# Performance work log

Hardware: AMD Instinct MI355X
Metric: run time of the kernel (lower is better)

The kernel has to match this reference:

```python
import jax, jax.numpy as jnp
import numpy as np

_EPSILON = 1e-6

def _sparsemax(z):
    # sparsemax along last axis. z: [b, m]
    z_sorted = -jnp.sort(-z, axis=-1)                       # descending sort
    m = z.shape[-1]
    k = jnp.arange(1, m + 1, dtype=z.dtype)                 # [m]
    z_cumsum = jnp.cumsum(z_sorted, axis=-1)                # [b, m]
    support = (1.0 + k * z_sorted) > z_cumsum               # [b, m] bool
    k_z = jnp.sum(support, axis=-1, keepdims=True)          # [b, 1] int, size of support
    cs_at_k = jnp.take_along_axis(z_cumsum, k_z - 1, axis=-1)
    tau = (cs_at_k - 1.0) / k_z.astype(z.dtype)             # threshold
    return jnp.maximum(z - tau, 0.0)


def setup_inputs() -> dict:
    key = jax.random.key(0)
    ks = jax.random.split(key, 6)
    b, m, dim, out_dim = 4096, 8192, 1024, 1000
    encoder_output = jax.random.normal(ks[0], (b, dim), dtype=jnp.float32)
    memory_set = jax.random.normal(ks[1], (m, dim), dtype=jnp.float32)
    loss_weights = jax.random.uniform(ks[2], (m, 1), dtype=jnp.float32)
    # classifier: Linear(2*dim, 4*dim) -> ReLU -> Linear(4*dim, out_dim)
    W1 = jax.random.normal(ks[3], (4 * dim, 2 * dim), dtype=jnp.float32) * (1.0 / np.sqrt(2 * dim))
    b1 = jnp.zeros((4 * dim,), dtype=jnp.float32)
    W2 = jax.random.normal(ks[4], (out_dim, 4 * dim), dtype=jnp.float32) * (1.0 / np.sqrt(4 * dim))
    b2 = jnp.zeros((out_dim,), dtype=jnp.float32)
    return {"encoder_output": encoder_output, "memory_set": memory_set,
            "loss_weights": loss_weights, "W1": W1, "b1": b1, "W2": W2, "b2": b2}


def reference(encoder_output, memory_set, loss_weights, W1, b1, W2, b2):
    # cosine distance: d = 1 - x_norm @ y_norm^T
    x_norm = encoder_output * jax.lax.rsqrt(
        jnp.sum(encoder_output * encoder_output, axis=1, keepdims=True) + _EPSILON)
    y_norm = memory_set * jax.lax.rsqrt(
        jnp.sum(memory_set * memory_set, axis=1, keepdims=True) + _EPSILON)
    d = 1.0 - jnp.matmul(x_norm, y_norm.T)                  # [b, m]
    content_weights = _sparsemax(-d)                        # [b, m], sparse rows
    memory_vector = jnp.matmul(content_weights, memory_set) # [b, dim]
    final_input = jnp.concatenate([encoder_output, memory_vector], axis=1)  # [b, 2*dim]
    h = jax.nn.relu(jnp.matmul(final_input, W1.T) + b1)
    output = jnp.matmul(h, W2.T) + b2                       # [b, out_dim]
    return output
```

## Files before the change

### kernel.cpp

```cpp
#include <hip/hip_runtime.h>

typedef __bf16 bf16;
typedef __bf16 bf16x4 __attribute__((ext_vector_type(4)));
typedef __bf16 bf16x8 __attribute__((ext_vector_type(8)));
typedef float f32x4 __attribute__((ext_vector_type(4)));
typedef _Float16 f16x8 __attribute__((ext_vector_type(8)));
typedef unsigned short ushort4v __attribute__((ext_vector_type(4)));

#define WS_OFF_S    (0ull)
#define WS_OFF_P4   (67108864ull)
#define WS_OFF_MB   (134217728ull)
#define WS_OFF_W1B  (150994944ull)
#define WS_OFF_W2B  (167772160ull)
#define WS_OFF_FI   (176160768ull)
#define WS_OFF_XN   (192937984ull)
#define WS_OFF_YN   (201326592ull)
#define WS_OFF_H    (0ull)

__device__ __forceinline__ void gload_lds16(const void* g, void* l) {
  __builtin_amdgcn_global_load_lds(
      (const __attribute__((address_space(1))) void*)g,
      (__attribute__((address_space(3))) void*)l, 16, 0, 0);
}

__device__ __forceinline__ f32x4 bf4_to_f32(bf16x4 v) {
  const ushort4v u = __builtin_bit_cast(ushort4v, v);
  f32x4 r;
#pragma unroll
  for (int k = 0; k < 4; ++k) {
    const unsigned q = ((unsigned)u[k]) << 16;
    r[k] = __builtin_bit_cast(float, q);
  }
  return r;
}

__device__ __forceinline__ float f16bits_to_f32(unsigned hb) {
  return (float)__builtin_bit_cast(_Float16, (unsigned short)hb);
}

template<int EPI>
__global__ __launch_bounds__(512, 2)
void gemm_nt256(const bf16* __restrict__ A, const bf16* __restrict__ B,
                void* __restrict__ Cout, const float* __restrict__ bias,
                int K, int ldab, int ldc)
{
  __shared__ alignas(16) bf16 As[2][256 * 64];
  __shared__ alignas(16) bf16 Bs[2][256 * 64];
  const int tid  = threadIdx.x;
  const int lane = tid & 63;
  const int wave = tid >> 6;
  const int wr = wave >> 2, wc = wave & 3;
  const int gx  = gridDim.x;
  const int nwg = gx * gridDim.y;
  int flat = blockIdx.y * gx + blockIdx.x;
  flat = (flat & 7) * (nwg >> 3) + (flat >> 3);
  const int bm0 = (flat / gx) << 8;
  const int bn0 = (flat % gx) << 8;
  const int zc  = blockIdx.z;

  const int lr    = lane >> 3;
  const int scolb = ((lane & 7) << 4) ^ (lr << 4);
  const int row0  = (wave << 5) + lr;
  const char* Ag = (const char*)(A + (size_t)(bm0 + row0) * ldab + (size_t)zc * K) + scolb;
  const char* Bg = (const char*)(B + (size_t)(bn0 + row0) * ldab + (size_t)zc * K) + scolb;
  char* Alds = (char*)As + (wave << 12);
  char* Blds = (char*)Bs + (wave << 12);
  const size_t rstride8 = (size_t)16 * ldab;

  int offA[2][8], offB[2][4];
  const int kb = (lane >> 4) << 4;
#pragma unroll
  for (int ks = 0; ks < 2; ++ks) {
#pragma unroll
    for (int m = 0; m < 8; ++m) {
      const int rA = (wr << 7) + (m << 4) + (lane & 15);
      offA[ks][m] = (rA << 7) + ((((ks << 6) + kb)) ^ ((rA & 7) << 4));
    }
#pragma unroll
    for (int n = 0; n < 4; ++n) {
      const int rB = (wc << 6) + (n << 4) + (lane & 15);
      offB[ks][n] = (rB << 7) + ((((ks << 6) + kb)) ^ ((rB & 7) << 4));
    }
  }

  f32x4 acc[8][4];
#pragma unroll
  for (int m = 0; m < 8; ++m)
#pragma unroll
    for (int n = 0; n < 4; ++n) acc[m][n] = (f32x4)(0.0f);

  auto STAGE = [&](int buf) {
    char* Ad = Alds + (buf << 15);
    char* Bd = Blds + (buf << 15);
#pragma unroll
    for (int i = 0; i < 4; ++i) gload_lds16(Ag + i * rstride8, Ad + (i << 10));
#pragma unroll
    for (int i = 0; i < 4; ++i) gload_lds16(Bg + i * rstride8, Bd + (i << 10));
    Ag += 128; Bg += 128;
  };

  const int nt = K >> 6;
  STAGE(0);
  STAGE(1);
  int cur = 0;
  for (int t = 0; t < nt; ++t) {
    if (t + 1 < nt) { asm volatile("s_waitcnt vmcnt(8)" ::: "memory"); }
    else            { asm volatile("s_waitcnt vmcnt(0)" ::: "memory"); }
    __builtin_amdgcn_s_barrier();
    asm volatile("" ::: "memory");
    const char* Ab = (const char*)As + (cur << 15);
    const char* Bb = (const char*)Bs + (cur << 15);
    __builtin_amdgcn_s_setprio(1);
#pragma unroll
    for (int ks = 0; ks < 2; ++ks) {
      bf16x8 av[8], bv[4];
#pragma unroll
      for (int m = 0; m < 8; ++m) av[m] = *(const bf16x8*)(Ab + offA[ks][m]);
#pragma unroll
      for (int n = 0; n < 4; ++n) bv[n] = *(const bf16x8*)(Bb + offB[ks][n]);
#pragma unroll
      for (int m = 0; m < 8; ++m)
#pragma unroll
        for (int n = 0; n < 4; ++n)
          acc[m][n] = __builtin_amdgcn_mfma_f32_16x16x32_bf16(av[m], bv[n], acc[m][n], 0, 0, 0);
    }
    __builtin_amdgcn_s_setprio(0);
    asm volatile("" ::: "memory");
    __builtin_amdgcn_s_barrier();
    if (t + 2 < nt) STAGE(cur);
    cur ^= 1;
  }

  const int r0 = bm0 + (wr << 7) + ((lane >> 4) << 2);
  const int c0 = bn0 + (wc << 6) + (lane & 15);
#pragma unroll
  for (int m = 0; m < 8; ++m) {
#pragma unroll
    for (int n = 0; n < 4; ++n) {
      const int col = c0 + (n << 4);
#pragma unroll
      for (int j = 0; j < 4; ++j) {
        const int row = r0 + (m << 4) + j;
        const float v = acc[m][n][j];
        if (EPI == 0) {
          ((_Float16*)Cout)[(size_t)row * ldc + col] = (_Float16)v;
        } else if (EPI == 2) {
          float t2 = v + bias[col];
          t2 = t2 > 0.f ? t2 : 0.f;
          ((bf16*)Cout)[(size_t)row * ldc + col] = (bf16)t2;
        } else {
          ((float*)Cout)[((size_t)zc << 22) + (size_t)row * ldc + col] = v;
        }
      }
    }
  }
}

__global__ __launch_bounds__(256)
void reduce_bias_kernel(const float* __restrict__ P4, const float* __restrict__ b2,
                        float* __restrict__ out)
{
  const int row = blockIdx.x;
  const int t = threadIdx.x;
  if (t >= 250) return;
  const size_t base = (size_t)row * 1024 + (t << 2);
  const float4 p0 = *(const float4*)(P4 + base);
  const float4 p1 = *(const float4*)(P4 + base + (1ull << 22));
  const float4 p2 = *(const float4*)(P4 + base + (2ull << 22));
  const float4 p3 = *(const float4*)(P4 + base + (3ull << 22));
  const float4 bb = ((const float4*)b2)[t];
  float4 r;
  r.x = p0.x + p1.x + p2.x + p3.x + bb.x;
  r.y = p0.y + p1.y + p2.y + p3.y + bb.y;
  r.z = p0.z + p1.z + p2.z + p3.z + bb.z;
  r.w = p0.w + p1.w + p2.w + p3.w + bb.w;
  *(float4*)(out + (size_t)row * 1000 + (t << 2)) = r;
}

__global__ __launch_bounds__(256)
void rownorm_kernel(const float* __restrict__ X, bf16* __restrict__ XN,
                    bf16* __restrict__ RAW, int ldraw)
{
  const int row = blockIdx.x;
  const int tid = threadIdx.x;
  const float4 v = ((const float4*)(X + (size_t)row * 1024))[tid];
  float ss = v.x * v.x + v.y * v.y + v.z * v.z + v.w * v.w;
#pragma unroll
  for (int o = 32; o > 0; o >>= 1) ss += __shfl_down(ss, o);
  __shared__ float red[4];
  if ((tid & 63) == 0) red[tid >> 6] = ss;
  __syncthreads();
  const float rn = rsqrtf(red[0] + red[1] + red[2] + red[3] + 1e-6f);
  union { bf16 h[4]; unsigned long long u; } p;
  p.h[0] = (bf16)(v.x * rn); p.h[1] = (bf16)(v.y * rn);
  p.h[2] = (bf16)(v.z * rn); p.h[3] = (bf16)(v.w * rn);
  ((unsigned long long*)(XN + (size_t)row * 1024))[tid] = p.u;
  if (RAW != nullptr) {
    union { bf16 h[4]; unsigned long long u; } q;
    q.h[0] = (bf16)v.x; q.h[1] = (bf16)v.y; q.h[2] = (bf16)v.z; q.h[3] = (bf16)v.w;
    ((unsigned long long*)(RAW + (size_t)row * ldraw))[tid] = q.u;
  }
}

__global__ void cvt_bf16_kernel(const float* __restrict__ src, bf16* __restrict__ dst, int n4) {
  const int i = blockIdx.x * blockDim.x + threadIdx.x;
  if (i >= n4) return;
  const float4 v = ((const float4*)src)[i];
  union { bf16 h[4]; unsigned long long u; } p;
  p.h[0] = (bf16)v.x; p.h[1] = (bf16)v.y; p.h[2] = (bf16)v.z; p.h[3] = (bf16)v.w;
  ((unsigned long long*)dst)[i] = p.u;
}

__global__ void cvt_w2_kernel(const float* __restrict__ src, bf16* __restrict__ dst) {
  const int i = blockIdx.x * blockDim.x + threadIdx.x;
  const int row = i >> 10;
  union { bf16 h[4]; unsigned long long u; } p;
  if (row < 1000) {
    const float4 v = ((const float4*)src)[i];
    p.h[0] = (bf16)v.x; p.h[1] = (bf16)v.y; p.h[2] = (bf16)v.z; p.h[3] = (bf16)v.w;
  } else {
    p.u = 0ull;
  }
  ((unsigned long long*)dst)[i] = p.u;
}

#define LCAP 1024
__global__ __launch_bounds__(256, 4)
void sparsemax_gather_kernel(const _Float16* __restrict__ S, const bf16* __restrict__ MB,
                             bf16* __restrict__ FI)
{
  const int row = blockIdx.x;
  const int tid = threadIdx.x;
  const f16x8* zs = (const f16x8*)(S + (size_t)row * 8192);
  float z[32];
  float lsum = 0.f;
#pragma unroll
  for (int t = 0; t < 4; ++t) {
    const f16x8 v = zs[t * 256 + tid];
#pragma unroll
    for (int j = 0; j < 8; ++j) { const float f = (float)v[j]; z[t * 8 + j] = f; lsum += f; }
  }
#pragma unroll
  for (int b = 0; b < 32; ++b) asm volatile("" : "+v"(z[b]));

  __shared__ float redS[4], redC[4];
  __shared__ unsigned pbuf[LCAP];
  __shared__ int lcnt;
  float s = lsum;
#pragma unroll
  for (int o = 32; o > 0; o >>= 1) s += __shfl_down(s, o);
  if ((tid & 63) == 0) redS[tid >> 6] = s;
  __syncthreads();
  float tau = (redS[0] + redS[1] + redS[2] + redS[3] - 1.0f) * (1.0f / 8192.0f);

  for (int it = 0; it < 64; ++it) {
    float ls = 0.f, lc = 0.f;
#pragma unroll
    for (int j = 0; j < 32; ++j) {
      const float v = z[j];
      if (v > tau) { ls += v; lc += 1.0f; }
    }
#pragma unroll
    for (int o = 32; o > 0; o >>= 1) { ls += __shfl_down(ls, o); lc += __shfl_down(lc, o); }
    __syncthreads();
    if ((tid & 63) == 0) { redS[tid >> 6] = ls; redC[tid >> 6] = lc; }
    __syncthreads();
    const float Ssum = redS[0] + redS[1] + redS[2] + redS[3];
    const float Csum = redC[0] + redC[1] + redC[2] + redC[3];
    const float ntau = (Ssum - 1.0f) / Csum;
    if (!(ntau > tau)) break;
    tau = ntau;
  }

  unsigned pend = 0;
#pragma unroll
  for (int b = 0; b < 32; ++b)
    if (z[b] > tau) pend |= (1u << b);

  const bf16* MBt = MB + (tid << 2);
  f32x4 acc0 = (f32x4)(0.0f), acc1 = (f32x4)(0.0f);
  for (;;) {
    if (tid == 0) lcnt = 0;
    __syncthreads();
#pragma unroll
    for (int b = 0; b < 32; ++b) {
      if (pend & (1u << b)) {
        const int slot = atomicAdd(&lcnt, 1);
        if (slot < LCAP) {
          const unsigned short wb =
              __builtin_bit_cast(unsigned short, (_Float16)(z[b] - tau));
          const unsigned idx = (unsigned)((((b >> 3) * 256 + tid) << 3) + (b & 7));
          pbuf[slot] = ((unsigned)wb << 16) | idx;
          pend &= ~(1u << b);
        }
      }
    }
    __syncthreads();
    const int nb = min(lcnt, LCAP);
    int e = 0;
    for (; e + 1 < nb; e += 2) {
      const uint2 pk2 = *(const uint2*)&pbuf[e];
      const float w0 = f16bits_to_f32(pk2.x >> 16);
      const float w1 = f16bits_to_f32(pk2.y >> 16);
      const bf16x4 v0 = *(const bf16x4*)(MBt + ((size_t)(pk2.x & 0xffffu) << 10));
      const bf16x4 v1 = *(const bf16x4*)(MBt + ((size_t)(pk2.y & 0xffffu) << 10));
      acc0 += bf4_to_f32(v0) * w0;
      acc1 += bf4_to_f32(v1) * w1;
    }
    if (e < nb) {
      const unsigned pk = pbuf[e];
      const float w = f16bits_to_f32(pk >> 16);
      const bf16x4 v = *(const bf16x4*)(MBt + ((size_t)(pk & 0xffffu) << 10));
      acc0 += bf4_to_f32(v) * w;
    }
    if (!__syncthreads_or(pend != 0)) break;
  }

  const f32x4 acc = acc0 + acc1;
  union { bf16 h[4]; unsigned long long u; } p;
  p.h[0] = (bf16)acc[0]; p.h[1] = (bf16)acc[1];
  p.h[2] = (bf16)acc[2]; p.h[3] = (bf16)acc[3];
  ((unsigned long long*)(FI + (size_t)row * 2048 + 1024))[tid] = p.u;
}

extern "C" void kernel_launch(void* const* d_in, const int* in_sizes, int n_in,
                              void* d_out, int out_size, void* d_ws, size_t ws_size,
                              hipStream_t stream)
{
  const float* enc = (const float*)d_in[0];
  const float* mem = (const float*)d_in[1];
  const float* W1  = (const float*)d_in[3];
  const float* b1  = (const float*)d_in[4];
  const float* W2  = (const float*)d_in[5];
  const float* b2  = (const float*)d_in[6];
  float* out = (float*)d_out;
  char* ws = (char*)d_ws;

  _Float16* S = (_Float16*)(ws + WS_OFF_S);
  float* P4 = (float*)(ws + WS_OFF_P4);
  bf16* MB  = (bf16*)(ws + WS_OFF_MB);
  bf16* W1B = (bf16*)(ws + WS_OFF_W1B);
  bf16* W2B = (bf16*)(ws + WS_OFF_W2B);
  bf16* FI  = (bf16*)(ws + WS_OFF_FI);
  bf16* XN  = (bf16*)(ws + WS_OFF_XN);
  bf16* YN  = (bf16*)(ws + WS_OFF_YN);
  bf16* H   = (bf16*)(ws + WS_OFF_H);

  rownorm_kernel<<<4096, 256, 0, stream>>>(enc, XN, FI, 2048);
  rownorm_kernel<<<8192, 256, 0, stream>>>(mem, YN, MB, 1024);
  cvt_bf16_kernel<<<8192, 256, 0, stream>>>(W1, W1B, 2097152);
  cvt_w2_kernel<<<4096, 256, 0, stream>>>(W2, W2B);

  gemm_nt256<0><<<dim3(32, 16), 512, 0, stream>>>(XN, YN, S, nullptr, 1024, 1024, 8192);
  sparsemax_gather_kernel<<<4096, 256, 0, stream>>>(S, MB, FI);
  gemm_nt256<2><<<dim3(16, 16), 512, 0, stream>>>(FI, W1B, H, b1, 2048, 2048, 4096);
  gemm_nt256<4><<<dim3(4, 16, 4), 512, 0, stream>>>(H, W2B, P4, nullptr, 1024, 4096, 1024);
  reduce_bias_kernel<<<4096, 256, 0, stream>>>(P4, b2, out);
}
```

Measured before the change: 447.7 us.

## Stage sparsemax row in LDS and warm-start tau from mean/std estimate

Measured after the change: 454.0 us. No clear change (+1.4%).

```diff
diff --git a/kernel.cpp b/kernel.cpp
--- a/kernel.cpp
+++ b/kernel.cpp
@@ -225,40 +225,50 @@
 }
 
 #define LCAP 1024
-__global__ __launch_bounds__(256, 4)
+__global__ __launch_bounds__(256, 6)
 void sparsemax_gather_kernel(const _Float16* __restrict__ S, const bf16* __restrict__ MB,
                              bf16* __restrict__ FI)
 {
   const int row = blockIdx.x;
   const int tid = threadIdx.x;
+
+  __shared__ alignas(16) unsigned short zl[8192];
+  __shared__ alignas(16) unsigned pbuf[LCAP];
+  __shared__ float redS[4], redC[4];
+  __shared__ int lcnt;
+  f16x8* zl8 = (f16x8*)zl;
+
   const f16x8* zs = (const f16x8*)(S + (size_t)row * 8192);
-  float z[32];
-  float lsum = 0.f;
+  float s1 = 0.f, s2 = 0.f;
 #pragma unroll
   for (int t = 0; t < 4; ++t) {
     const f16x8 v = zs[t * 256 + tid];
-#pragma unroll
-    for (int j = 0; j < 8; ++j) { const float f = (float)v[j]; z[t * 8 + j] = f; lsum += f; }
-  }
-#pragma unroll
-  for (int b = 0; b < 32; ++b) asm volatile("" : "+v"(z[b]));
-
-  __shared__ float redS[4], redC[4];
-  __shared__ unsigned pbuf[LCAP];
-  __shared__ int lcnt;
-  float s = lsum;
-#pragma unroll
-  for (int o = 32; o > 0; o >>= 1) s += __shfl_down(s, o);
-  if ((tid & 63) == 0) redS[tid >> 6] = s;
+    zl8[t * 256 + tid] = v;
+#pragma unroll
+    for (int j = 0; j < 8; ++j) { const float f = (float)v[j]; s1 += f; s2 += f * f; }
+  }
+#pragma unroll
+  for (int o = 32; o > 0; o >>= 1) { s1 += __shfl_down(s1, o); s2 += __shfl_down(s2, o); }
+  if ((tid & 63) == 0) { redS[tid >> 6] = s1; redC[tid >> 6] = s2; }
   __syncthreads();
-  float tau = (redS[0] + redS[1] + redS[2] + redS[3] - 1.0f) * (1.0f / 8192.0f);
+  const float Stot  = redS[0] + redS[1] + redS[2] + redS[3];
+  const float S2tot = redC[0] + redC[1] + redC[2] + redC[3];
+  const float mu = Stot * (1.0f / 8192.0f);
+  float var = S2tot * (1.0f / 8192.0f) - mu * mu;
+  var = var > 0.f ? var : 0.f;
+  const float coldTau = (Stot - 1.0f) * (1.0f / 8192.0f);
+  float tau = mu + 1.8f * sqrtf(var);
 
   for (int it = 0; it < 64; ++it) {
     float ls = 0.f, lc = 0.f;
 #pragma unroll
-    for (int j = 0; j < 32; ++j) {
-      const float v = z[j];
-      if (v > tau) { ls += v; lc += 1.0f; }
+    for (int t = 0; t < 4; ++t) {
+      const f16x8 v = zl8[t * 256 + tid];
+#pragma unroll
+      for (int j = 0; j < 8; ++j) {
+        const float f = (float)v[j];
+        if (f > tau) { ls += f; lc += 1.0f; }
+      }
     }
 #pragma unroll
     for (int o = 32; o > 0; o >>= 1) { ls += __shfl_down(ls, o); lc += __shfl_down(lc, o); }
@@ -267,35 +277,40 @@
     __syncthreads();
     const float Ssum = redS[0] + redS[1] + redS[2] + redS[3];
     const float Csum = redC[0] + redC[1] + redC[2] + redC[3];
+    if (Csum == 0.f) { tau = coldTau; continue; }
     const float ntau = (Ssum - 1.0f) / Csum;
-    if (!(ntau > tau)) break;
-    tau = ntau;
-  }
-
-  unsigned pend = 0;
-#pragma unroll
-  for (int b = 0; b < 32; ++b)
-    if (z[b] > tau) pend |= (1u << b);
+    if (ntau > tau) { tau = ntau; continue; }
+    if (it == 0 && ntau < tau) { tau = coldTau; continue; }
+    break;
+  }
 
   const bf16* MBt = MB + (tid << 2);
   f32x4 acc0 = (f32x4)(0.0f), acc1 = (f32x4)(0.0f);
-  for (;;) {
-    if (tid == 0) lcnt = 0;
-    __syncthreads();
-#pragma unroll
-    for (int b = 0; b < 32; ++b) {
-      if (pend & (1u << b)) {
+  unsigned pend = 0;
+
+  if (tid == 0) lcnt = 0;
+  __syncthreads();
+#pragma unroll
+  for (int t = 0; t < 4; ++t) {
+    const f16x8 v = zl8[t * 256 + tid];
+#pragma unroll
+    for (int j = 0; j < 8; ++j) {
+      const float w = (float)v[j] - tau;
+      if (w > 0.f) {
         const int slot = atomicAdd(&lcnt, 1);
         if (slot < LCAP) {
-          const unsigned short wb =
-              __builtin_bit_cast(unsigned short, (_Float16)(z[b] - tau));
-          const unsigned idx = (unsigned)((((b >> 3) * 256 + tid) << 3) + (b & 7));
+          const unsigned short wb = __builtin_bit_cast(unsigned short, (_Float16)w);
+          const unsigned idx = (unsigned)(((t * 256 + tid) << 3) + j);
           pbuf[slot] = ((unsigned)wb << 16) | idx;
-          pend &= ~(1u << b);
+        } else {
+          pend |= (1u << (t * 8 + j));
         }
       }
     }
-    __syncthreads();
+  }
+  __syncthreads();
+
+  for (;;) {
     const int nb = min(lcnt, LCAP);
     int e = 0;
     for (; e + 1 < nb; e += 2) {
@@ -314,6 +329,23 @@
       acc0 += bf4_to_f32(v) * w;
     }
     if (!__syncthreads_or(pend != 0)) break;
+    if (tid == 0) lcnt = 0;
+    __syncthreads();
+#pragma unroll
+    for (int b = 0; b < 32; ++b) {
+      if (pend & (1u << b)) {
+        const unsigned idx = (unsigned)((((b >> 3) * 256 + tid) << 3) + (b & 7));
+        const float zv = (float)__builtin_bit_cast(_Float16, zl[idx]);
+        const float w = zv - tau;
+        const int slot = atomicAdd(&lcnt, 1);
+        if (slot < LCAP) {
+          const unsigned short wb = __builtin_bit_cast(unsigned short, (_Float16)w);
+          pbuf[slot] = ((unsigned)wb << 16) | idx;
+          pend &= ~(1u << b);
+        }
+      }
+    }
+    __syncthreads();
   }
 
   const f32x4 acc = acc0 + acc1;
```
